# Performance work log

Measured on AMD Instinct MI355X. Metric: run time of the kernel, lower is better.

## Reference

```python
import jax, jax.numpy as jnp
import numpy as np

N, D = 8192, 1024
NUM_CLASSES = 128
PPC = 4  # prototypes per class
P = NUM_CLASSES * PPC
ALPHA = 1.0
EPS = 1e-9


def setup_inputs() -> dict:
    key = jax.random.key(0)
    k1, k2, k3 = jax.random.split(key, 3)
    x = jax.random.normal(k1, (N, D), dtype=jnp.float32)
    y = jax.random.randint(k2, (N,), 0, NUM_CLASSES, dtype=jnp.int64)
    prototypes = jax.random.normal(k3, (P, D), dtype=jnp.float32)
    return {"x": x, "y": y, "t_value": 1, "prototypes": prototypes}


def reference(x, y, t_value, prototypes):
    # prototype labels: i // PPC
    proto_labels = jnp.arange(P, dtype=y.dtype) // PPC  # [P]

    x_sq = jnp.sum(x * x, axis=1, keepdims=True)          # [N,1]
    p_sq = jnp.sum(prototypes * prototypes, axis=1)       # [P]
    dist = x_sq + p_sq[None, :] - 2.0 * (x @ prototypes.T)  # [N,P]

    correct_mask = proto_labels[None, :] == y[:, None]    # [N,P]
    inf = jnp.array(jnp.inf, dtype=dist.dtype)
    d1 = jnp.min(jnp.where(correct_mask, dist, inf), axis=1)   # [N]
    d2 = jnp.min(jnp.where(correct_mask, inf, dist), axis=1)   # [N]

    mu = (d1 - d2) / (d1 + d2 + EPS)
    alpha = jnp.log(1.0 + jnp.asarray(t_value, dtype=dist.dtype)) / ALPHA
    return jnp.mean(jax.nn.sigmoid(alpha * mu))
```

## Files before the change

### kernel.cpp

```cpp
#include <hip/hip_runtime.h>
#include <hip/hip_bf16.h>
#include <math.h>
#include <stdint.h>

#define NS 8192
#define DD 1024
#define NP 512
#define NPARTS 16
#define EPSF 1e-9f
#define BIGF 3.0e38f

typedef __attribute__((ext_vector_type(8))) short bf16x8;
typedef __attribute__((ext_vector_type(4))) float f32x4;

__device__ inline unsigned short f32_to_bf16(float f) {
    uint32_t u = __builtin_bit_cast(uint32_t, f);
    uint32_t r = (u + 0x7FFFu + ((u >> 16) & 1u)) >> 16;
    return (unsigned short)r;
}

__global__ __launch_bounds__(256) void prep_kernel(
    const float* __restrict__ x, const float* __restrict__ protos,
    unsigned short* __restrict__ xb, unsigned short* __restrict__ pb,
    float* __restrict__ xsq, float* __restrict__ psq)
{
    int row = blockIdx.x;
    const float* src;
    unsigned short* dstb;
    float* dsts;
    if (row < NS) {
        src = x + (size_t)row * DD; dstb = xb + (size_t)row * DD; dsts = xsq + row;
    } else {
        int r = row - NS;
        src = protos + (size_t)r * DD; dstb = pb + (size_t)r * DD; dsts = psq + r;
    }
    int t = threadIdx.x;
    float4 v = ((const float4*)src)[t];
    float ss = v.x * v.x + v.y * v.y + v.z * v.z + v.w * v.w;
    ushort4 o;
    o.x = f32_to_bf16(v.x); o.y = f32_to_bf16(v.y);
    o.z = f32_to_bf16(v.z); o.w = f32_to_bf16(v.w);
    ((ushort4*)dstb)[t] = o;
    for (int off = 32; off; off >>= 1) ss += __shfl_down(ss, off);
    __shared__ float red[4];
    if ((t & 63) == 0) red[t >> 6] = ss;
    __syncthreads();
    if (t == 0) dsts[0] = red[0] + red[1] + red[2] + red[3];
}

__global__ __launch_bounds__(256) void glvq_gemm(
    const unsigned short* __restrict__ Xb, const unsigned short* __restrict__ Pb,
    const float* __restrict__ xsq, const float* __restrict__ psq,
    const int* __restrict__ y,
    float* __restrict__ d1p, float* __restrict__ d2p)
{
    __shared__ unsigned short As[64 * 64];
    __shared__ unsigned short Bs[64 * 64];

    const int tid  = threadIdx.x;
    const int lane = tid & 63;
    const int wid  = tid >> 6;
    const int wr = wid >> 1, wc = wid & 1;

    const int d    = blockIdx.x;
    const int xcd  = d & 7;
    const int slot = d >> 3;
    const int mb   = xcd * 16 + (slot & 15);
    const int nb   = slot >> 4;
    const int m0   = mb * 64;
    const int n0   = nb * 64;

    const int srow   = lane >> 3;
    const int scol16 = (lane & 7) ^ srow;
    const int sub = lane & 15, g = lane >> 4;

    f32x4 acc[2][2] = {};

    for (int kt = 0; kt < DD / 64; ++kt) {
        const int k0 = kt * 64;
#pragma unroll
        for (int j = 0; j < 2; ++j) {
            const int row = j * 32 + wid * 8;
            const unsigned short* ga = Xb + (size_t)(m0 + row + srow) * DD + k0 + scol16 * 8;
            const unsigned short* gb = Pb + (size_t)(n0 + row + srow) * DD + k0 + scol16 * 8;
            __builtin_amdgcn_global_load_lds(
                (const __attribute__((address_space(1))) void*)ga,
                (__attribute__((address_space(3))) void*)((char*)As + row * 128), 16, 0, 0);
            __builtin_amdgcn_global_load_lds(
                (const __attribute__((address_space(1))) void*)gb,
                (__attribute__((address_space(3))) void*)((char*)Bs + row * 128), 16, 0, 0);
        }
        __syncthreads();

#pragma unroll
        for (int kk = 0; kk < 2; ++kk) {
            bf16x8 a[2], b[2];
#pragma unroll
            for (int m = 0; m < 2; ++m) {
                const int row = wr * 32 + m * 16 + sub;
                const int c16 = (kk * 4 + g) ^ (row & 7);
                a[m] = *(const bf16x8*)((const char*)As + row * 128 + c16 * 16);
            }
#pragma unroll
            for (int n = 0; n < 2; ++n) {
                const int row = wc * 32 + n * 16 + sub;
                const int c16 = (kk * 4 + g) ^ (row & 7);
                b[n] = *(const bf16x8*)((const char*)Bs + row * 128 + c16 * 16);
            }
#pragma unroll
            for (int m = 0; m < 2; ++m)
#pragma unroll
                for (int n = 0; n < 2; ++n)
                    acc[m][n] = __builtin_amdgcn_mfma_f32_16x16x32_bf16(a[m], b[n], acc[m][n], 0, 0, 0);
        }
        __syncthreads();
    }

    float psqv[2];
    int   lab[2];
#pragma unroll
    for (int n = 0; n < 2; ++n) {
        const int col = n0 + wc * 32 + n * 16 + sub;
        psqv[n] = psq[col];
        lab[n]  = col >> 2;
    }
    const int part = nb * 2 + wc;
#pragma unroll
    for (int m = 0; m < 2; ++m) {
#pragma unroll
        for (int r = 0; r < 4; ++r) {
            const int row = m0 + wr * 32 + m * 16 + g * 4 + r;
            const float xs = xsq[row];
            const int yy = y[row];
            float d1 = BIGF, d2 = BIGF;
#pragma unroll
            for (int n = 0; n < 2; ++n) {
                const float dist = xs + psqv[n] - 2.0f * acc[m][n][r];
                if (lab[n] == yy) d1 = fminf(d1, dist);
                else              d2 = fminf(d2, dist);
            }
            for (int off = 8; off; off >>= 1) {
                d1 = fminf(d1, __shfl_xor(d1, off));
                d2 = fminf(d2, __shfl_xor(d2, off));
            }
            if (sub == 0) {
                d1p[part * NS + row] = d1;
                d2p[part * NS + row] = d2;
            }
        }
    }
}

__global__ __launch_bounds__(256) void finalize_kernel(
    const float* __restrict__ d1p, const float* __restrict__ d2p,
    const int* __restrict__ tval, float* __restrict__ bsum)
{
    const int row = blockIdx.x * 256 + threadIdx.x;
    float d1 = BIGF, d2 = BIGF;
#pragma unroll
    for (int p = 0; p < NPARTS; ++p) {
        d1 = fminf(d1, d1p[p * NS + row]);
        d2 = fminf(d2, d2p[p * NS + row]);
    }
    const float mu = (d1 - d2) / (d1 + d2 + EPSF);
    const float alpha = logf(1.0f + (float)tval[0]);
    float s = 1.0f / (1.0f + expf(-alpha * mu));
    for (int off = 32; off; off >>= 1) s += __shfl_down(s, off);
    __shared__ float red[4];
    if ((threadIdx.x & 63) == 0) red[threadIdx.x >> 6] = s;
    __syncthreads();
    if (threadIdx.x == 0) bsum[blockIdx.x] = red[0] + red[1] + red[2] + red[3];
}

__global__ void final_sum(const float* __restrict__ bsum, float* __restrict__ out) {
    float s = (threadIdx.x < NS / 256) ? bsum[threadIdx.x] : 0.0f;
    for (int off = 32; off; off >>= 1) s += __shfl_down(s, off);
    if (threadIdx.x == 0) out[0] = s * (1.0f / (float)NS);
}

extern "C" void kernel_launch(void* const* d_in, const int* in_sizes, int n_in,
                              void* d_out, int out_size, void* d_ws, size_t ws_size,
                              hipStream_t stream) {
    const float* x      = (const float*)d_in[0];
    const int*   y      = (const int*)d_in[1];
    const int*   tval   = (const int*)d_in[2];
    const float* protos = (const float*)d_in[3];
    float* out = (float*)d_out;

    char* ws = (char*)d_ws;
    unsigned short* xb  = (unsigned short*)(ws);
    unsigned short* pb  = (unsigned short*)(ws + (size_t)NS * DD * 2);
    float* xsq  = (float*)(ws + (size_t)(NS + NP) * DD * 2);
    float* psq  = (float*)(ws + (size_t)(NS + NP) * DD * 2 + NS * 4);
    float* d1p  = (float*)(ws + (size_t)(NS + NP) * DD * 2 + (NS + NP) * 4);
    float* d2p  = d1p + (size_t)NPARTS * NS;
    float* bsum = d2p + (size_t)NPARTS * NS;

    prep_kernel<<<NS + NP, 256, 0, stream>>>(x, protos, xb, pb, xsq, psq);
    glvq_gemm<<<(NS / 64) * (NP / 64), 256, 0, stream>>>(xb, pb, xsq, psq, y, d1p, d2p);
    finalize_kernel<<<NS / 256, 256, 0, stream>>>(d1p, d2p, tval, bsum);
    final_sum<<<1, 64, 0, stream>>>(bsum, out);
}
```

Baseline: 37.86 us.

## Double-buffer LDS tiles and widen GEMM N-tile to 128 prototypes

The GEMM kernel now stages the next K-tile into a second LDS buffer while computing on the current one, removing one barrier per iteration. It also widens each block's prototype tile from 64 to 128, so each wave computes a 2x4 set of MFMA tiles and the X tile is reused across more columns. The number of partial-min partitions halves accordingly. This uses more LDS and registers per block and launches half as many blocks (512), which may lower occupancy and leave CUs underfilled.

Measured after the change: 37.41 us. No clear change (-1.2%).

```diff
diff --git a/kernel.cpp b/kernel.cpp
--- a/kernel.cpp
+++ b/kernel.cpp
@@ -6,7 +6,7 @@
 #define NS 8192
 #define DD 1024
 #define NP 512
-#define NPARTS 16
+#define NPARTS 8
 #define EPSF 1e-9f
 #define BIGF 3.0e38f
 
@@ -54,8 +54,8 @@
     const int* __restrict__ y,
     float* __restrict__ d1p, float* __restrict__ d2p)
 {
-    __shared__ unsigned short As[64 * 64];
-    __shared__ unsigned short Bs[64 * 64];
+    __shared__ unsigned short As[2][64 * 64];
+    __shared__ unsigned short Bs[2][128 * 64];
 
     const int tid  = threadIdx.x;
     const int lane = tid & 63;
@@ -68,59 +68,75 @@
     const int mb   = xcd * 16 + (slot & 15);
     const int nb   = slot >> 4;
     const int m0   = mb * 64;
-    const int n0   = nb * 64;
+    const int n0   = nb * 128;
 
     const int srow   = lane >> 3;
     const int scol16 = (lane & 7) ^ srow;
     const int sub = lane & 15, g = lane >> 4;
 
-    f32x4 acc[2][2] = {};
-
-    for (int kt = 0; kt < DD / 64; ++kt) {
+    f32x4 acc[2][4] = {};
+
+    auto stage = [&](int buf, int kt) {
         const int k0 = kt * 64;
 #pragma unroll
         for (int j = 0; j < 2; ++j) {
-            const int row = j * 32 + wid * 8;
-            const unsigned short* ga = Xb + (size_t)(m0 + row + srow) * DD + k0 + scol16 * 8;
-            const unsigned short* gb = Pb + (size_t)(n0 + row + srow) * DD + k0 + scol16 * 8;
+            const int c = wid * 2 + j;
+            const unsigned short* ga = Xb + (size_t)(m0 + c * 8 + srow) * DD + k0 + scol16 * 8;
             __builtin_amdgcn_global_load_lds(
                 (const __attribute__((address_space(1))) void*)ga,
-                (__attribute__((address_space(3))) void*)((char*)As + row * 128), 16, 0, 0);
+                (__attribute__((address_space(3))) void*)((char*)&As[buf][0] + c * 1024), 16, 0, 0);
+        }
+#pragma unroll
+        for (int j = 0; j < 4; ++j) {
+            const int c = wid * 4 + j;
+            const unsigned short* gb = Pb + (size_t)(n0 + c * 8 + srow) * DD + k0 + scol16 * 8;
             __builtin_amdgcn_global_load_lds(
                 (const __attribute__((address_space(1))) void*)gb,
-                (__attribute__((address_space(3))) void*)((char*)Bs + row * 128), 16, 0, 0);
-        }
-        __syncthreads();
-
+                (__attribute__((address_space(3))) void*)((char*)&Bs[buf][0] + c * 1024), 16, 0, 0);
+        }
+    };
+
+    auto compute = [&](int buf) {
 #pragma unroll
         for (int kk = 0; kk < 2; ++kk) {
-            bf16x8 a[2], b[2];
+            bf16x8 a[2], b[4];
 #pragma unroll
             for (int m = 0; m < 2; ++m) {
                 const int row = wr * 32 + m * 16 + sub;
                 const int c16 = (kk * 4 + g) ^ (row & 7);
-                a[m] = *(const bf16x8*)((const char*)As + row * 128 + c16 * 16);
-            }
-#pragma unroll
-            for (int n = 0; n < 2; ++n) {
-                const int row = wc * 32 + n * 16 + sub;
+                a[m] = *(const bf16x8*)((const char*)&As[buf][0] + row * 128 + c16 * 16);
+            }
+#pragma unroll
+            for (int n = 0; n < 4; ++n) {
+                const int row = wc * 64 + n * 16 + sub;
                 const int c16 = (kk * 4 + g) ^ (row & 7);
-                b[n] = *(const bf16x8*)((const char*)Bs + row * 128 + c16 * 16);
+                b[n] = *(const bf16x8*)((const char*)&Bs[buf][0] + row * 128 + c16 * 16);
             }
 #pragma unroll
             for (int m = 0; m < 2; ++m)
 #pragma unroll
-                for (int n = 0; n < 2; ++n)
+                for (int n = 0; n < 4; ++n)
                     acc[m][n] = __builtin_amdgcn_mfma_f32_16x16x32_bf16(a[m], b[n], acc[m][n], 0, 0, 0);
         }
+    };
+
+    stage(0, 0);
+    __syncthreads();
+    int cur = 0;
+#pragma unroll 1
+    for (int kt = 0; kt < DD / 64 - 1; ++kt) {
+        stage(cur ^ 1, kt + 1);
+        compute(cur);
         __syncthreads();
-    }
-
-    float psqv[2];
-    int   lab[2];
-#pragma unroll
-    for (int n = 0; n < 2; ++n) {
-        const int col = n0 + wc * 32 + n * 16 + sub;
+        cur ^= 1;
+    }
+    compute(cur);
+
+    float psqv[4];
+    int   lab[4];
+#pragma unroll
+    for (int n = 0; n < 4; ++n) {
+        const int col = n0 + wc * 64 + n * 16 + sub;
         psqv[n] = psq[col];
         lab[n]  = col >> 2;
     }
@@ -134,7 +150,7 @@
             const int yy = y[row];
             float d1 = BIGF, d2 = BIGF;
 #pragma unroll
-            for (int n = 0; n < 2; ++n) {
+            for (int n = 0; n < 4; ++n) {
                 const float dist = xs + psqv[n] - 2.0f * acc[m][n][r];
                 if (lab[n] == yy) d1 = fminf(d1, dist);
                 else              d2 = fminf(d2, dist);
@@ -197,7 +213,7 @@
     float* bsum = d2p + (size_t)NPARTS * NS;
 
     prep_kernel<<<NS + NP, 256, 0, stream>>>(x, protos, xb, pb, xsq, psq);
-    glvq_gemm<<<(NS / 64) * (NP / 64), 256, 0, stream>>>(xb, pb, xsq, psq, y, d1p, d2p);
+    glvq_gemm<<<(NS / 64) * (NP / 128), 256, 0, stream>>>(xb, pb, xsq, psq, y, d1p, d2p);
     finalize_kernel<<<NS / 256, 256, 0, stream>>>(d1p, d2p, tval, bsum);
     final_sum<<<1, 64, 0, stream>>>(bsum, out);
 }
```

## Restructure GEMM: 128x64 tiles, direct-global A loads, double-buffered K=256 B stages

Applied to the files above, without the earlier changes.

The GEMM kernel now uses 512-thread blocks with 128x64 output tiles. Each wave reads its X fragments directly from global memory instead of staging them in LDS. Prototype tiles are staged through double-buffered LDS in four K-chunks of 256, so the copy of the next chunk overlaps with MFMA work on the current one. Per-block partial minima are merged in LDS before being written, which halves the number of partitions finalize has to read. The trade-off is uncoalesced global A reads that rely on the cache, and fewer blocks in flight.

New measurement: 59.06 us. 1.56x slower.

```diff
diff --git a/kernel.cpp b/kernel.cpp
--- a/kernel.cpp
+++ b/kernel.cpp
@@ -6,7 +6,10 @@
 #define NS 8192
 #define DD 1024
 #define NP 512
-#define NPARTS 16
+#define MT 128
+#define NT 64
+#define KQ 256
+#define NPARTS 8
 #define EPSF 1e-9f
 #define BIGF 3.0e38f
 
@@ -48,73 +51,71 @@
     if (t == 0) dsts[0] = red[0] + red[1] + red[2] + red[3];
 }
 
-__global__ __launch_bounds__(256) void glvq_gemm(
-    const unsigned short* __restrict__ Xb, const unsigned short* __restrict__ Pb,
+__global__ __launch_bounds__(512, 2) void glvq_fused(
+    const unsigned short* __restrict__ xb, const unsigned short* __restrict__ pb,
     const float* __restrict__ xsq, const float* __restrict__ psq,
     const int* __restrict__ y,
     float* __restrict__ d1p, float* __restrict__ d2p)
 {
-    __shared__ unsigned short As[64 * 64];
-    __shared__ unsigned short Bs[64 * 64];
+    __shared__ unsigned short Bs[2][NT * KQ];
+    __shared__ float dpart[MT][2][2];
 
     const int tid  = threadIdx.x;
     const int lane = tid & 63;
     const int wid  = tid >> 6;
-    const int wr = wid >> 1, wc = wid & 1;
-
+    const int wg   = wid >> 1;
+    const int wc   = wid & 1;
     const int d    = blockIdx.x;
     const int xcd  = d & 7;
     const int slot = d >> 3;
-    const int mb   = xcd * 16 + (slot & 15);
-    const int nb   = slot >> 4;
-    const int m0   = mb * 64;
-    const int n0   = nb * 64;
-
-    const int srow   = lane >> 3;
-    const int scol16 = (lane & 7) ^ srow;
-    const int sub = lane & 15, g = lane >> 4;
+    const int mb   = xcd * 8 + (slot & 7);
+    const int nb   = slot >> 3;
+    const int m0   = mb * MT;
+    const int n0   = nb * NT;
+    const int sub  = lane & 15, g = lane >> 4;
 
     f32x4 acc[2][2] = {};
 
-    for (int kt = 0; kt < DD / 64; ++kt) {
-        const int k0 = kt * 64;
-#pragma unroll
-        for (int j = 0; j < 2; ++j) {
-            const int row = j * 32 + wid * 8;
-            const unsigned short* ga = Xb + (size_t)(m0 + row + srow) * DD + k0 + scol16 * 8;
-            const unsigned short* gb = Pb + (size_t)(n0 + row + srow) * DD + k0 + scol16 * 8;
+    auto stage = [&](int buf, int q) {
+#pragma unroll
+        for (int j = 0; j < 4; ++j) {
+            const int rbase = wid * 8 + j * 2;
+            const int row   = rbase + (lane >> 5);
+            const int sc    = (lane & 31) ^ (row & 15);
+            const unsigned short* gp = pb + (size_t)(n0 + row) * DD + q * KQ + sc * 8;
             __builtin_amdgcn_global_load_lds(
-                (const __attribute__((address_space(1))) void*)ga,
-                (__attribute__((address_space(3))) void*)((char*)As + row * 128), 16, 0, 0);
-            __builtin_amdgcn_global_load_lds(
-                (const __attribute__((address_space(1))) void*)gb,
-                (__attribute__((address_space(3))) void*)((char*)Bs + row * 128), 16, 0, 0);
+                (const __attribute__((address_space(1))) void*)gp,
+                (__attribute__((address_space(3))) void*)((char*)&Bs[buf][0] + rbase * 512),
+                16, 0, 0);
         }
-        __syncthreads();
-
-#pragma unroll
-        for (int kk = 0; kk < 2; ++kk) {
-            bf16x8 a[2], b[2];
-#pragma unroll
-            for (int m = 0; m < 2; ++m) {
-                const int row = wr * 32 + m * 16 + sub;
-                const int c16 = (kk * 4 + g) ^ (row & 7);
-                a[m] = *(const bf16x8*)((const char*)As + row * 128 + c16 * 16);
-            }
-#pragma unroll
-            for (int n = 0; n < 2; ++n) {
-                const int row = wc * 32 + n * 16 + sub;
-                const int c16 = (kk * 4 + g) ^ (row & 7);
-                b[n] = *(const bf16x8*)((const char*)Bs + row * 128 + c16 * 16);
-            }
-#pragma unroll
-            for (int m = 0; m < 2; ++m)
-#pragma unroll
-                for (int n = 0; n < 2; ++n)
-                    acc[m][n] = __builtin_amdgcn_mfma_f32_16x16x32_bf16(a[m], b[n], acc[m][n], 0, 0, 0);
+    };
+
+    const unsigned short* xr0 = xb + (size_t)(m0 + wg * 32 + sub) * DD;
+    const unsigned short* xr1 = xr0 + (size_t)16 * DD;
+
+    auto computeQ = [&](int buf, int q) {
+#pragma unroll
+        for (int kt = 0; kt < KQ / 32; ++kt) {
+            bf16x8 a0 = *(const bf16x8*)(xr0 + q * KQ + kt * 32 + g * 8);
+            bf16x8 a1 = *(const bf16x8*)(xr1 + q * KQ + kt * 32 + g * 8);
+            const int c    = kt * 4 + g;
+            const int col0 = wc * 32 + sub;
+            const int col1 = wc * 32 + 16 + sub;
+            bf16x8 b0 = *(const bf16x8*)((const char*)&Bs[buf][0] + col0 * 512 + ((c ^ (col0 & 15)) * 16));
+            bf16x8 b1 = *(const bf16x8*)((const char*)&Bs[buf][0] + col1 * 512 + ((c ^ (col1 & 15)) * 16));
+            acc[0][0] = __builtin_amdgcn_mfma_f32_16x16x32_bf16(a0, b0, acc[0][0], 0, 0, 0);
+            acc[0][1] = __builtin_amdgcn_mfma_f32_16x16x32_bf16(a0, b1, acc[0][1], 0, 0, 0);
+            acc[1][0] = __builtin_amdgcn_mfma_f32_16x16x32_bf16(a1, b0, acc[1][0], 0, 0, 0);
+            acc[1][1] = __builtin_amdgcn_mfma_f32_16x16x32_bf16(a1, b1, acc[1][1], 0, 0, 0);
         }
-        __syncthreads();
-    }
+    };
+
+    stage(0, 0);
+    __syncthreads();
+    stage(1, 1); computeQ(0, 0); __syncthreads();
+    stage(0, 2); computeQ(1, 1); __syncthreads();
+    stage(1, 3); computeQ(0, 2); __syncthreads();
+    computeQ(1, 3);
 
     float psqv[2];
     int   lab[2];
@@ -124,14 +125,13 @@
         psqv[n] = psq[col];
         lab[n]  = col >> 2;
     }
-    const int part = nb * 2 + wc;
 #pragma unroll
     for (int m = 0; m < 2; ++m) {
 #pragma unroll
         for (int r = 0; r < 4; ++r) {
-            const int row = m0 + wr * 32 + m * 16 + g * 4 + r;
-            const float xs = xsq[row];
-            const int yy = y[row];
+            const int rl = wg * 32 + m * 16 + g * 4 + r;
+            const float xs = xsq[m0 + rl];
+            const int yy = y[m0 + rl];
             float d1 = BIGF, d2 = BIGF;
 #pragma unroll
             for (int n = 0; n < 2; ++n) {
@@ -143,11 +143,13 @@
                 d1 = fminf(d1, __shfl_xor(d1, off));
                 d2 = fminf(d2, __shfl_xor(d2, off));
             }
-            if (sub == 0) {
-                d1p[part * NS + row] = d1;
-                d2p[part * NS + row] = d2;
-            }
+            if (sub == 0) { dpart[rl][wc][0] = d1; dpart[rl][wc][1] = d2; }
         }
+    }
+    __syncthreads();
+    if (tid < MT) {
+        d1p[nb * NS + m0 + tid] = fminf(dpart[tid][0][0], dpart[tid][1][0]);
+        d2p[nb * NS + m0 + tid] = fminf(dpart[tid][0][1], dpart[tid][1][1]);
     }
 }
 
@@ -188,8 +190,8 @@
     float* out = (float*)d_out;
 
     char* ws = (char*)d_ws;
-    unsigned short* xb  = (unsigned short*)(ws);
-    unsigned short* pb  = (unsigned short*)(ws + (size_t)NS * DD * 2);
+    unsigned short* xb = (unsigned short*)(ws);
+    unsigned short* pb = (unsigned short*)(ws + (size_t)NS * DD * 2);
     float* xsq  = (float*)(ws + (size_t)(NS + NP) * DD * 2);
     float* psq  = (float*)(ws + (size_t)(NS + NP) * DD * 2 + NS * 4);
     float* d1p  = (float*)(ws + (size_t)(NS + NP) * DD * 2 + (NS + NP) * 4);
@@ -197,7 +199,7 @@
     float* bsum = d2p + (size_t)NPARTS * NS;
 
     prep_kernel<<<NS + NP, 256, 0, stream>>>(x, protos, xb, pb, xsq, psq);
-    glvq_gemm<<<(NS / 64) * (NP / 64), 256, 0, stream>>>(xb, pb, xsq, psq, y, d1p, d2p);
+    glvq_fused<<<(NS / MT) * (NP / NT), 512, 0, stream>>>(xb, pb, xsq, psq, y, d1p, d2p);
     finalize_kernel<<<NS / 256, 256, 0, stream>>>(d1p, d2p, tval, bsum);
     final_sum<<<1, 64, 0, stream>>>(bsum, out);
 }
```
